# Optimization experiments

Hardware: AMD Instinct MI355X
Metric: run time of the kernel (lower is better)

The kernel has to match this reference:

```python
import jax, jax.numpy as jnp
import numpy as np

B = 262144
STEPS = 15            # Program.steps = var(15)
SPEED = 5.0           # Program.straight_speed
TRAJ_IDX = np.array([10, 1, 2, 3, 4, 5, 6, 7, 8, 17])
FEAT_IDX = np.array([1, 2, 3, 4, 9, 17])


def setup_inputs() -> dict:
    key = jax.random.key(0)
    ks = jax.random.split(key, 9)
    x = jax.random.normal(ks[0], (B, 18), dtype=jnp.float32)
    x = x.at[:, 0].set(0.0)  # loop counter i starts at 0 -> exactly 15 iterations
    return {
        "x": x,
        "c1w": jax.random.normal(ks[1], (2,), jnp.float32) * 0.5,
        "c1b": jax.random.normal(ks[2], (1,), jnp.float32) * 0.1,
        "c2w": jax.random.normal(ks[3], (2,), jnp.float32) * 0.5,
        "c2b": jax.random.normal(ks[4], (1,), jnp.float32) * 0.1,
        "l1w": jax.random.normal(ks[5], (4, 32), jnp.float32) * 0.3,
        "l1b": jax.random.normal(ks[6], (32,), jnp.float32) * 0.1,
        "l2w": jax.random.normal(ks[7], (32, 5), jnp.float32) * 0.3,
        "l2b": jax.random.normal(ks[8], (5,), jnp.float32) * 0.1,
    }


def _classifier(feat, c1w, c1b, c2w, c2b, l1w, l1b, l2w, l2b):
    # feat: [B,6] -> conv1d(k=2): [B,5] -> conv1d(k=2): [B,4] -> 32 -> 5, sigmoid
    h = jax.nn.relu(c1w[0] * feat[:, :-1] + c1w[1] * feat[:, 1:] + c1b)
    h = jax.nn.relu(c2w[0] * h[:, :-1] + c2w[1] * h[:, 1:] + c2b)
    h = jax.nn.relu(h @ l1w + l1b)
    return jax.nn.sigmoid(h @ l2w + l2b)  # [B,5]


def _distance(s):
    return (s[:, 1] - s[:, 3]) ** 2 + (s[:, 2] - s[:, 4]) ** 2


def _program(x, c1w, c1b, c2w, c2b, l1w, l1b, l2w, l2b):
    s = x.at[:, 10].set(_distance(x))          # initial assign_distance
    traj0 = s[:, TRAJ_IDX]                      # initial trajectory_update

    def step(s, _):
        # assign_branch_probability
        p = _classifier(s[:, FEAT_IDX], c1w, c1b, c2w, c2b, l1w, l1b, l2w, l2b)
        s = (s.at[:, 5].set(p[:, 0]).at[:, 6].set(p[:, 1]).at[:, 7].set(p[:, 2])
              .at[:, 8].set(p[:, 3]).at[:, 17].set(p[:, 4]))
        p5, p6, p7, p8 = p[:, 0], p[:, 1], p[:, 2], p[:, 3]
        # assign_comparison_block: pairwise diffs a..f at indices 11..16
        a, b, c = p6 - p5, p7 - p5, p8 - p5
        d, e, f = p7 - p6, p8 - p6, p8 - p7
        s = (s.at[:, 11].set(a).at[:, 12].set(b).at[:, 13].set(c)
              .at[:, 14].set(d).at[:, 15].set(e).at[:, 16].set(f))
        # ifelse_argmax_ITE: nested compare against comparison_bar=0.0
        dx_c = jnp.where(c <= 0.0, 0.0, SPEED);  st_c = jnp.where(c <= 0.0, 0.0, 3.0)   # cruise vs right
        dx_f = jnp.where(f <= 0.0, 0.0, SPEED);  st_f = jnp.where(f <= 0.0, 2.0, 3.0)   # straight vs right
        dx_e = jnp.where(e <= 0.0, -SPEED, SPEED); st_e = jnp.where(e <= 0.0, 1.0, 3.0)  # left vs right
        dx_b = jnp.where(b <= 0.0, dx_c, dx_f);  st_b = jnp.where(b <= 0.0, st_c, st_f)
        dx_d = jnp.where(d <= 0.0, dx_e, dx_f);  st_d = jnp.where(d <= 0.0, st_e, st_f)
        dx   = jnp.where(a <= 0.0, dx_b, dx_d);  st   = jnp.where(a <= 0.0, st_b, st_d)
        s = s.at[:, 1].add(dx).at[:, 9].set(st)
        # assign_y1, assign_x2, assign_update_i, assign_distance
        s = s.at[:, 2].add(SPEED).at[:, 3].add(SPEED).at[:, 0].add(1.0)
        s = s.at[:, 10].set(_distance(s))
        return s, s[:, TRAJ_IDX]

    s, recs = jax.lax.scan(step, s, None, length=STEPS)
    traj = jnp.concatenate([traj0[:, None, :], jnp.moveaxis(recs, 0, 1)], axis=1)  # [B,16,10]
    return jnp.concatenate([s, traj.reshape(s.shape[0], -1)], axis=1)  # [B, 18+160]


def reference(x, c1w, c1b, c2w, c2b, l1w, l1b, l2w, l2b):
    return _program(x, c1w, c1b, c2w, c2b, l1w, l1b, l2w, l2b)
```

## Files before the change

kernel.cpp:

```cpp
#include <hip/hip_runtime.h>


constexpr int kB     = 262144;
constexpr int kSteps = 15;
constexpr int PAD    = 33;
constexpr int RPB    = 128;
constexpr int WOFF   = RPB * PAD;

__device__ __forceinline__ float relu_(float v) { return fmaxf(v, 0.0f); }
__device__ __forceinline__ float sigmoid_(float v) {
    return __builtin_amdgcn_rcpf(1.0f + __expf(-v));
}

__global__ __launch_bounds__(256, 2) void Program_4578435138231_kernel(
    const float* __restrict__ x,
    const float* __restrict__ c1w, const float* __restrict__ c1b,
    const float* __restrict__ c2w, const float* __restrict__ c2b,
    const float* __restrict__ l1w, const float* __restrict__ l1b,
    const float* __restrict__ l2w, const float* __restrict__ l2b,
    float* __restrict__ out)
{
    __shared__ __align__(16) float lds[RPB * PAD + 32 * 12];
    const int tid  = threadIdx.x;
    const int rid  = tid >> 1;
    const int half = tid & 1;
    const int R0   = blockIdx.x * RPB;

    if (tid < 32) {
        const int k = tid;
        float* w = lds + WOFF + k * 12;
        w[0] = l1w[k];          w[1] = l1w[32 + k];
        w[2] = l1w[64 + k];     w[3] = l1w[96 + k];
        w[4] = l1b[k];
        w[5] = l2w[5 * k + 0];  w[6] = l2w[5 * k + 1];
        w[7] = l2w[5 * k + 2];  w[8] = l2w[5 * k + 3];
        w[9] = l2w[5 * k + 4];
    }

    {
        const float* xblk = x + (size_t)R0 * 18;
        #pragma unroll
        for (int j = 0; j < 9; ++j) {
            int flat = tid + 256 * j;
            float v  = xblk[flat];
            int r = (int)(((unsigned)flat * 58255u) >> 20);
            int c = flat - r * 18;
            lds[r * PAD + c] = v;
        }
    }
    __syncthreads();
    float s[18];
    #pragma unroll
    for (int j = 0; j < 18; ++j) s[j] = lds[rid * PAD + j];

    const float* wl = lds + WOFF + half * (16 * 12);
    float wA[16], wB[16], wC[16], wD[16], wE[16];
    float wF[16], wG[16], wH[16], wI[16], wJ[16];
    #pragma unroll
    for (int k = 0; k < 16; ++k) {
        float4 a = *reinterpret_cast<const float4*>(wl + k * 12);
        float4 b = *reinterpret_cast<const float4*>(wl + k * 12 + 4);
        float2 c = *reinterpret_cast<const float2*>(wl + k * 12 + 8);
        wA[k] = a.x; wB[k] = a.y; wC[k] = a.z; wD[k] = a.w; wE[k] = b.x;
        wF[k] = b.y; wG[k] = b.z; wH[k] = b.w; wI[k] = c.x; wJ[k] = c.y;
    }
    #pragma unroll
    for (int k = 0; k < 16; ++k) {
        asm volatile("" : "+v"(wA[k]), "+v"(wB[k]), "+v"(wC[k]), "+v"(wD[k]),
                          "+v"(wE[k]), "+v"(wF[k]), "+v"(wG[k]), "+v"(wH[k]),
                          "+v"(wI[k]), "+v"(wJ[k]));
    }
    __syncthreads();

    const float cw10 = c1w[0], cw11 = c1w[1], cb1 = c1b[0];
    const float cw20 = c2w[0], cw21 = c2w[1], cb2 = c2b[0];
    const float b20 = half ? 0.f : l2b[0], b21 = half ? 0.f : l2b[1];
    const float b22 = half ? 0.f : l2b[2], b23 = half ? 0.f : l2b[3];
    const float b24 = half ? 0.f : l2b[4];

    {
        float dA = s[1] - s[3], dB = s[2] - s[4];
        s[10] = dA * dA + dB * dB;
    }

    float* lr = lds + rid * PAD;
    auto rec = [&](int idx, float v) { if (!half) lr[idx] = v; };

    auto flush32 = [&](int wcol) {
        __syncthreads();
        const int rr = tid >> 5, cc = tid & 31;
        const float* lp = lds + rr * PAD + cc;
        float*       op = out + (size_t)(R0 + rr) * 178 + wcol + cc;
        #pragma unroll
        for (int j = 0; j < 16; ++j) {
            op[(size_t)(8 * j) * 178] = lp[8 * j * PAD];
        }
        __syncthreads();
    };

    int wstart = 18;
    int nextb  = 50;

    rec(0, s[10]); rec(1, s[1]);  rec(2, s[2]); rec(3, s[3]); rec(4, s[4]);
    rec(5, s[5]);  rec(6, s[6]);  rec(7, s[7]); rec(8, s[8]); rec(9, s[17]);

    #pragma unroll 1
    for (int t = 0; t < kSteps; ++t) {
        float f0 = s[1], f1 = s[2], f2 = s[3], f3 = s[4], f4 = s[9], f5 = s[17];
        float h10 = relu_(cw10 * f0 + cw11 * f1 + cb1);
        float h11 = relu_(cw10 * f1 + cw11 * f2 + cb1);
        float h12 = relu_(cw10 * f2 + cw11 * f3 + cb1);
        float h13 = relu_(cw10 * f3 + cw11 * f4 + cb1);
        float h14 = relu_(cw10 * f4 + cw11 * f5 + cb1);
        float g0 = relu_(cw20 * h10 + cw21 * h11 + cb2);
        float g1 = relu_(cw20 * h11 + cw21 * h12 + cb2);
        float g2 = relu_(cw20 * h12 + cw21 * h13 + cb2);
        float g3 = relu_(cw20 * h13 + cw21 * h14 + cb2);

        float p0 = b20, p1 = b21, p2 = b22, p3 = b23, p4 = b24;
        #pragma unroll
        for (int k = 0; k < 16; ++k) {
            float h = g0 * wA[k] + g1 * wB[k] + g2 * wC[k]
                    + g3 * wD[k] + wE[k];
            h = relu_(h);
            p0 += h * wF[k];
            p1 += h * wG[k];
            p2 += h * wH[k];
            p3 += h * wI[k];
            p4 += h * wJ[k];
        }
        p0 += __shfl_xor(p0, 1, 64);
        p1 += __shfl_xor(p1, 1, 64);
        p2 += __shfl_xor(p2, 1, 64);
        p3 += __shfl_xor(p3, 1, 64);
        p4 += __shfl_xor(p4, 1, 64);

        p0 = sigmoid_(p0); p1 = sigmoid_(p1); p2 = sigmoid_(p2);
        p3 = sigmoid_(p3); p4 = sigmoid_(p4);

        s[5] = p0; s[6] = p1; s[7] = p2; s[8] = p3; s[17] = p4;
        float a = p1 - p0, b = p2 - p0, c = p3 - p0;
        float d = p2 - p1, e = p3 - p1, f = p3 - p2;
        s[11] = a; s[12] = b; s[13] = c; s[14] = d; s[15] = e; s[16] = f;

        float dx_c = (c <= 0.f) ? 0.f  : 5.f,  st_c = (c <= 0.f) ? 0.f : 3.f;
        float dx_f = (f <= 0.f) ? 0.f  : 5.f,  st_f = (f <= 0.f) ? 2.f : 3.f;
        float dx_e = (e <= 0.f) ? -5.f : 5.f,  st_e = (e <= 0.f) ? 1.f : 3.f;
        float dx_b = (b <= 0.f) ? dx_c : dx_f, st_b = (b <= 0.f) ? st_c : st_f;
        float dx_d = (d <= 0.f) ? dx_e : dx_f, st_d = (d <= 0.f) ? st_e : st_f;
        float dx   = (a <= 0.f) ? dx_b : dx_d, st   = (a <= 0.f) ? st_b : st_d;

        s[1] += dx; s[9] = st;
        s[2] += 5.f; s[3] += 5.f; s[0] += 1.f;
        float dA = s[1] - s[3], dB = s[2] - s[4];
        s[10] = dA * dA + dB * dB;

        float v0 = s[10], v1 = s[1], v2 = s[2], v3 = s[3], v4 = s[4];
        float v5 = s[5],  v6 = s[6], v7 = s[7], v8 = s[8], v9 = s[17];
        const int c0 = 28 + 10 * t;
        const int kk = nextb - c0;
        int off = c0 - wstart;
        if (kk >= 10) {
            rec(off + 0, v0); rec(off + 1, v1); rec(off + 2, v2);
            rec(off + 3, v3); rec(off + 4, v4); rec(off + 5, v5);
            rec(off + 6, v6); rec(off + 7, v7); rec(off + 8, v8);
            rec(off + 9, v9);
            if (kk == 10) {
                flush32(wstart);
                wstart = nextb; nextb += 32;
            }
        } else {
            if (kk > 0) rec(off + 0, v0);
            if (kk > 1) rec(off + 1, v1);
            if (kk > 2) rec(off + 2, v2);
            if (kk > 3) rec(off + 3, v3);
            if (kk > 4) rec(off + 4, v4);
            if (kk > 5) rec(off + 5, v5);
            if (kk > 6) rec(off + 6, v6);
            if (kk > 7) rec(off + 7, v7);
            if (kk > 8) rec(off + 8, v8);
            if (kk > 9) rec(off + 9, v9);
            flush32(wstart);
            wstart = nextb; nextb += 32;
            off = c0 - wstart;
            if (kk <= 0) rec(off + 0, v0);
            if (kk <= 1) rec(off + 1, v1);
            if (kk <= 2) rec(off + 2, v2);
            if (kk <= 3) rec(off + 3, v3);
            if (kk <= 4) rec(off + 4, v4);
            if (kk <= 5) rec(off + 5, v5);
            if (kk <= 6) rec(off + 6, v6);
            if (kk <= 7) rec(off + 7, v7);
            if (kk <= 8) rec(off + 8, v8);
            if (kk <= 9) rec(off + 9, v9);
        }
    }

    __syncthreads();
    if (!half) {
        #pragma unroll
        for (int j = 0; j < 18; ++j) lr[j] = s[j];
    }
    __syncthreads();
    #pragma unroll
    for (int j = 0; j < 9; ++j) {
        int flat = tid + 256 * j;
        int r = (int)(((unsigned)flat * 58255u) >> 20);
        int c = flat - r * 18;
        out[(size_t)(R0 + r) * 178 + c] = lds[r * PAD + c];
    }
}

extern "C" void kernel_launch(void* const* d_in, const int* in_sizes, int n_in,
                              void* d_out, int out_size, void* d_ws, size_t ws_size,
                              hipStream_t stream) {
    const float* x   = (const float*)d_in[0];
    const float* c1w = (const float*)d_in[1];
    const float* c1b = (const float*)d_in[2];
    const float* c2w = (const float*)d_in[3];
    const float* c2b = (const float*)d_in[4];
    const float* l1w = (const float*)d_in[5];
    const float* l1b = (const float*)d_in[6];
    const float* l2w = (const float*)d_in[7];
    const float* l2b = (const float*)d_in[8];
    float* out = (float*)d_out;

    Program_4578435138231_kernel<<<kB / RPB, 256, 0, stream>>>(
        x, c1w, c1b, c2w, c2b, l1w, l1b, l2w, l2b, out);
}
```

Baseline: 267.8 us.

## Keep MLP weights in lane registers via readlane and split hidden units across half-blocks

Each thread now holds a single weight slice per lane instead of 160 register-resident weights, and fetches each hidden unit's weights with readlane broadcasts. Hidden units are split between the low and high 128 threads, which hold the same rows, so the partial sums are combined through LDS with two block barriers per step instead of a lane shuffle. The output staging window shrinks from 32 to 16 columns and the padded x staging is replaced by a flat copy. The aim is to cut register pressure and raise occupancy. In exchange it adds per-step block-wide syncs, more frequent flushes and scalar readlane traffic.

```diff
diff --git a/kernel.cpp b/kernel.cpp
--- a/kernel.cpp
+++ b/kernel.cpp
@@ -3,16 +3,21 @@
 
 constexpr int kB     = 262144;
 constexpr int kSteps = 15;
-constexpr int PAD    = 33;
+constexpr int PAD    = 17;
 constexpr int RPB    = 128;
-constexpr int WOFF   = RPB * PAD;
+constexpr int WIN    = RPB * PAD;
+constexpr int XOFF   = WIN;
+constexpr int WSTG   = WIN + 1280;
 
 __device__ __forceinline__ float relu_(float v) { return fmaxf(v, 0.0f); }
 __device__ __forceinline__ float sigmoid_(float v) {
     return __builtin_amdgcn_rcpf(1.0f + __expf(-v));
 }
-
-__global__ __launch_bounds__(256, 2) void Program_4578435138231_kernel(
+__device__ __forceinline__ float rl_(float v, int lane) {
+    return __int_as_float(__builtin_amdgcn_readlane(__float_as_int(v), lane));
+}
+
+__global__ __launch_bounds__(256) void Program_4578435138231_kernel(
     const float* __restrict__ x,
     const float* __restrict__ c1w, const float* __restrict__ c1b,
     const float* __restrict__ c2w, const float* __restrict__ c2b,
@@ -20,21 +25,25 @@
     const float* __restrict__ l2w, const float* __restrict__ l2b,
     float* __restrict__ out)
 {
-    __shared__ __align__(16) float lds[RPB * PAD + 32 * 12];
+    __shared__ __align__(16) float lds[WSTG + 320];
     const int tid  = threadIdx.x;
-    const int rid  = tid >> 1;
-    const int half = tid & 1;
+    const int r    = tid & 127;
+    const bool isLow = (tid & 128) == 0;
     const int R0   = blockIdx.x * RPB;
 
     if (tid < 32) {
         const int k = tid;
-        float* w = lds + WOFF + k * 12;
-        w[0] = l1w[k];          w[1] = l1w[32 + k];
-        w[2] = l1w[64 + k];     w[3] = l1w[96 + k];
-        w[4] = l1b[k];
-        w[5] = l2w[5 * k + 0];  w[6] = l2w[5 * k + 1];
-        w[7] = l2w[5 * k + 2];  w[8] = l2w[5 * k + 3];
-        w[9] = l2w[5 * k + 4];
+        float* w = lds + WSTG;
+        w[0 * 32 + k] = l1w[k];
+        w[1 * 32 + k] = l1w[32 + k];
+        w[2 * 32 + k] = l1w[64 + k];
+        w[3 * 32 + k] = l1w[96 + k];
+        w[4 * 32 + k] = l1b[k];
+        w[5 * 32 + k] = l2w[5 * k + 0];
+        w[6 * 32 + k] = l2w[5 * k + 1];
+        w[7 * 32 + k] = l2w[5 * k + 2];
+        w[8 * 32 + k] = l2w[5 * k + 3];
+        w[9 * 32 + k] = l2w[5 * k + 4];
     }
 
     {
@@ -42,64 +51,55 @@
         #pragma unroll
         for (int j = 0; j < 9; ++j) {
             int flat = tid + 256 * j;
-            float v  = xblk[flat];
-            int r = (int)(((unsigned)flat * 58255u) >> 20);
-            int c = flat - r * 18;
-            lds[r * PAD + c] = v;
+            lds[flat] = xblk[flat];
         }
     }
     __syncthreads();
     float s[18];
     #pragma unroll
-    for (int j = 0; j < 18; ++j) s[j] = lds[rid * PAD + j];
-
-    const float* wl = lds + WOFF + half * (16 * 12);
-    float wA[16], wB[16], wC[16], wD[16], wE[16];
-    float wF[16], wG[16], wH[16], wI[16], wJ[16];
-    #pragma unroll
-    for (int k = 0; k < 16; ++k) {
-        float4 a = *reinterpret_cast<const float4*>(wl + k * 12);
-        float4 b = *reinterpret_cast<const float4*>(wl + k * 12 + 4);
-        float2 c = *reinterpret_cast<const float2*>(wl + k * 12 + 8);
-        wA[k] = a.x; wB[k] = a.y; wC[k] = a.z; wD[k] = a.w; wE[k] = b.x;
-        wF[k] = b.y; wG[k] = b.z; wH[k] = b.w; wI[k] = c.x; wJ[k] = c.y;
-    }
-    #pragma unroll
-    for (int k = 0; k < 16; ++k) {
-        asm volatile("" : "+v"(wA[k]), "+v"(wB[k]), "+v"(wC[k]), "+v"(wD[k]),
-                          "+v"(wE[k]), "+v"(wF[k]), "+v"(wG[k]), "+v"(wH[k]),
-                          "+v"(wI[k]), "+v"(wJ[k]));
-    }
+    for (int j = 0; j < 18; ++j) s[j] = lds[r * 18 + j];
+
+    const float* wl = lds + WSTG;
+    const int lk = tid & 31;
+    float w0 = wl[0 * 32 + lk], w1 = wl[1 * 32 + lk], w2 = wl[2 * 32 + lk];
+    float w3 = wl[3 * 32 + lk], w4 = wl[4 * 32 + lk], w5 = wl[5 * 32 + lk];
+    float w6 = wl[6 * 32 + lk], w7 = wl[7 * 32 + lk], w8 = wl[8 * 32 + lk];
+    float w9 = wl[9 * 32 + lk];
+    asm volatile("" : "+v"(w0), "+v"(w1), "+v"(w2), "+v"(w3), "+v"(w4),
+                      "+v"(w5), "+v"(w6), "+v"(w7), "+v"(w8), "+v"(w9));
+    const int kbase = __builtin_amdgcn_readfirstlane((tid & 128) >> 3);
     __syncthreads();
 
     const float cw10 = c1w[0], cw11 = c1w[1], cb1 = c1b[0];
     const float cw20 = c2w[0], cw21 = c2w[1], cb2 = c2b[0];
-    const float b20 = half ? 0.f : l2b[0], b21 = half ? 0.f : l2b[1];
-    const float b22 = half ? 0.f : l2b[2], b23 = half ? 0.f : l2b[3];
-    const float b24 = half ? 0.f : l2b[4];
+    const float b20 = l2b[0], b21 = l2b[1], b22 = l2b[2], b23 = l2b[3], b24 = l2b[4];
 
     {
         float dA = s[1] - s[3], dB = s[2] - s[4];
         s[10] = dA * dA + dB * dB;
     }
 
-    float* lr = lds + rid * PAD;
-    auto rec = [&](int idx, float v) { if (!half) lr[idx] = v; };
-
-    auto flush32 = [&](int wcol) {
-        __syncthreads();
-        const int rr = tid >> 5, cc = tid & 31;
+    float* lr  = lds + r * PAD;
+    float* exW = lds + XOFF + (tid & 255) * 0;
+    float* exMine  = lds + XOFF + ((isLow ? 0 : 128) + r) * 5;
+    const float* exOther = lds + XOFF + ((isLow ? 128 : 0) + r) * 5;
+
+    auto rec = [&](int idx, float v) { if (isLow) lr[idx] = v; };
+
+    auto flush16 = [&](int wcol) {
+        __syncthreads();
+        const int rr = tid >> 4, cc = tid & 15;
         const float* lp = lds + rr * PAD + cc;
         float*       op = out + (size_t)(R0 + rr) * 178 + wcol + cc;
         #pragma unroll
-        for (int j = 0; j < 16; ++j) {
-            op[(size_t)(8 * j) * 178] = lp[8 * j * PAD];
+        for (int j = 0; j < 8; ++j) {
+            op[(size_t)(16 * j) * 178] = lp[16 * j * PAD];
         }
         __syncthreads();
     };
 
     int wstart = 18;
-    int nextb  = 50;
+    int nextb  = 34;
 
     rec(0, s[10]); rec(1, s[1]);  rec(2, s[2]); rec(3, s[3]); rec(4, s[4]);
     rec(5, s[5]);  rec(6, s[6]);  rec(7, s[7]); rec(8, s[8]); rec(9, s[17]);
@@ -117,23 +117,28 @@
         float g2 = relu_(cw20 * h12 + cw21 * h13 + cb2);
         float g3 = relu_(cw20 * h13 + cw21 * h14 + cb2);
 
-        float p0 = b20, p1 = b21, p2 = b22, p3 = b23, p4 = b24;
-        #pragma unroll
-        for (int k = 0; k < 16; ++k) {
-            float h = g0 * wA[k] + g1 * wB[k] + g2 * wC[k]
-                    + g3 * wD[k] + wE[k];
+        float p0 = isLow ? b20 : 0.f, p1 = isLow ? b21 : 0.f;
+        float p2 = isLow ? b22 : 0.f, p3 = isLow ? b23 : 0.f;
+        float p4 = isLow ? b24 : 0.f;
+        #pragma unroll
+        for (int i = 0; i < 16; ++i) {
+            const int kk_ = kbase + i;
+            float h = g0 * rl_(w0, kk_) + g1 * rl_(w1, kk_)
+                    + g2 * rl_(w2, kk_) + g3 * rl_(w3, kk_) + rl_(w4, kk_);
             h = relu_(h);
-            p0 += h * wF[k];
-            p1 += h * wG[k];
-            p2 += h * wH[k];
-            p3 += h * wI[k];
-            p4 += h * wJ[k];
-        }
-        p0 += __shfl_xor(p0, 1, 64);
-        p1 += __shfl_xor(p1, 1, 64);
-        p2 += __shfl_xor(p2, 1, 64);
-        p3 += __shfl_xor(p3, 1, 64);
-        p4 += __shfl_xor(p4, 1, 64);
+            p0 += h * rl_(w5, kk_);
+            p1 += h * rl_(w6, kk_);
+            p2 += h * rl_(w7, kk_);
+            p3 += h * rl_(w8, kk_);
+            p4 += h * rl_(w9, kk_);
+        }
+
+        exMine[0] = p0; exMine[1] = p1; exMine[2] = p2;
+        exMine[3] = p3; exMine[4] = p4;
+        __syncthreads();
+        p0 += exOther[0]; p1 += exOther[1]; p2 += exOther[2];
+        p3 += exOther[3]; p4 += exOther[4];
+        __syncthreads();
 
         p0 = sigmoid_(p0); p1 = sigmoid_(p1); p2 = sigmoid_(p2);
         p3 = sigmoid_(p3); p4 = sigmoid_(p4);
@@ -166,8 +171,8 @@
             rec(off + 6, v6); rec(off + 7, v7); rec(off + 8, v8);
             rec(off + 9, v9);
             if (kk == 10) {
-                flush32(wstart);
-                wstart = nextb; nextb += 32;
+                flush16(wstart);
+                wstart = nextb; nextb += 16;
             }
         } else {
             if (kk > 0) rec(off + 0, v0);
@@ -180,8 +185,8 @@
             if (kk > 7) rec(off + 7, v7);
             if (kk > 8) rec(off + 8, v8);
             if (kk > 9) rec(off + 9, v9);
-            flush32(wstart);
-            wstart = nextb; nextb += 32;
+            flush16(wstart);
+            wstart = nextb; nextb += 16;
             off = c0 - wstart;
             if (kk <= 0) rec(off + 0, v0);
             if (kk <= 1) rec(off + 1, v1);
@@ -197,17 +202,17 @@
     }
 
     __syncthreads();
-    if (!half) {
-        #pragma unroll
-        for (int j = 0; j < 18; ++j) lr[j] = s[j];
+    if (isLow) {
+        #pragma unroll
+        for (int j = 0; j < 18; ++j) lds[r * 18 + j] = s[j];
     }
     __syncthreads();
     #pragma unroll
     for (int j = 0; j < 9; ++j) {
         int flat = tid + 256 * j;
-        int r = (int)(((unsigned)flat * 58255u) >> 20);
-        int c = flat - r * 18;
-        out[(size_t)(R0 + r) * 178 + c] = lds[r * PAD + c];
+        int rr = (int)(((unsigned)flat * 58255u) >> 20);
+        int cc = flat - rr * 18;
+        out[(size_t)(R0 + rr) * 178 + cc] = lds[flat];
     }
 }
 
```

New measurement: 310.2 us. 15.8% more time.
